# Kernel tuning notes

Measured on AMD Instinct MI355X. Metric: run time of the kernel, lower is better.

## Reference

```python
import jax, jax.numpy as jnp
import numpy as np

B, T, D_IN = 8192, 32, 2
EMB, H = 128, 256


def setup_inputs() -> dict:
    key = jax.random.key(0)
    ks = jax.random.split(key, 8)
    s = 0.05
    return {
        "traj_inputs": jax.random.normal(ks[0], (B, T, D_IN), dtype=jnp.float32),
        "W_emb": jax.random.normal(ks[1], (D_IN, EMB), dtype=jnp.float32) * s,
        "b_emb": jnp.zeros((EMB,), dtype=jnp.float32),
        "W0": jax.random.normal(ks[2], (EMB, 4 * H), dtype=jnp.float32) * s,
        "U0": jax.random.normal(ks[3], (H, 4 * H), dtype=jnp.float32) * s,
        "b0": jnp.zeros((4 * H,), dtype=jnp.float32),
        "W1": jax.random.normal(ks[4], (H, 4 * H), dtype=jnp.float32) * s,
        "U1": jax.random.normal(ks[5], (H, 4 * H), dtype=jnp.float32) * s,
        "b1": jnp.zeros((4 * H,), dtype=jnp.float32),
    }


def _lstm_layer(x_seq, W, U, b):
    # x_seq: [B, T, D]; Keras LSTMCell gate order i, f, g(c), o
    bsz = x_seq.shape[0]
    h0 = jnp.zeros((bsz, H), dtype=x_seq.dtype)
    c0 = jnp.zeros((bsz, H), dtype=x_seq.dtype)
    # precompute input projection for all timesteps (one big GEMM)
    xz = jnp.einsum("btd,dk->btk", x_seq, W) + b  # [B, T, 4H]

    def step(carry, xz_t):
        h, c = carry
        z = xz_t + h @ U
        i, f, g, o = jnp.split(z, 4, axis=-1)
        i = jax.nn.sigmoid(i)
        f = jax.nn.sigmoid(f)
        g = jnp.tanh(g)
        o = jax.nn.sigmoid(o)
        c = f * c + i * g
        h = o * jnp.tanh(c)
        return (h, c), h

    (h_f, c_f), ys = jax.lax.scan(step, (h0, c0), jnp.swapaxes(xz, 0, 1))
    return jnp.swapaxes(ys, 0, 1), h_f, c_f  # [B,T,H], [B,H], [B,H]


def reference(traj_inputs, W_emb, b_emb, W0, U0, b0, W1, U1, b1):
    # position embedding: Dense(emb_size, relu)
    x = jax.nn.relu(traj_inputs @ W_emb + b_emb)  # [B, T, EMB]
    # stacked 2-layer LSTM, return_sequences + return_state
    y0, h0, c0 = _lstm_layer(x, W0, U0, b0)
    y1, h1, c1 = _lstm_layer(y0, W1, U1, b1)
    # Keras RNN(StackedRNNCells) returns (seq_out, [h0,c0], [h1,c1])
    return y1, h0, c0, h1, c1
```

## Files before the change

kernel.cpp:

```cpp
#include <hip/hip_runtime.h>
#include <hip/hip_bf16.h>


typedef __attribute__((ext_vector_type(8))) __bf16 bf16x8;
typedef __attribute__((ext_vector_type(4))) __bf16 bf16x4;
typedef __attribute__((ext_vector_type(4))) float f32x4;

#define MFMA16(a, b, c) __builtin_amdgcn_mfma_f32_16x16x32_bf16(a, b, c, 0, 0, 0)

#define WAIT_VM3() __builtin_amdgcn_s_waitcnt(0xF73)
#define WAIT_LGKM0() __builtin_amdgcn_s_waitcnt(0xC07F)
#define RAW_BARRIER()                  \
  do {                                 \
    WAIT_LGKM0();                      \
    __builtin_amdgcn_sched_barrier(0); \
    __builtin_amdgcn_s_barrier();      \
  } while (0)

__device__ __forceinline__ float fexp2(float x) {
#if __has_builtin(__builtin_amdgcn_exp2f)
  return __builtin_amdgcn_exp2f(x);
#else
  return exp2f(x);
#endif
}
__device__ __forceinline__ float frcp(float x) {
#if __has_builtin(__builtin_amdgcn_rcpf)
  return __builtin_amdgcn_rcpf(x);
#else
  return 1.0f / x;
#endif
}
__device__ __forceinline__ float fsig(float x) {
  return frcp(1.0f + fexp2(-1.44269504f * x));
}
__device__ __forceinline__ float ftanh(float x) {
  return 1.0f - 2.0f * frcp(1.0f + fexp2(2.88539008f * x));
}

__global__ void prep_w0(const float* __restrict__ W0, const float* __restrict__ U0,
                        __bf16* __restrict__ o) {
  const int f = blockIdx.x * 256 + threadIdx.x;
  const int j = f & 7, l5 = (f >> 3) & 63, g = f >> 9;
  const int kc = g % 12, q = (g / 12) & 3, wid = g / 48;
  const int k = (kc << 5) + ((l5 >> 4) << 3) + j;
  const int c = (q << 8) + ((wid >> 2) << 6) + ((wid & 3) << 4) + (l5 & 15);
  const float v = (k < 128) ? W0[(k << 10) + c] : U0[((k - 128) << 10) + c];
  o[f] = (__bf16)v;
}
__global__ void prep_w1(const float* __restrict__ W1, const float* __restrict__ U1,
                        __bf16* __restrict__ o) {
  const int f = blockIdx.x * 256 + threadIdx.x;
  const int j = f & 7, l5 = (f >> 3) & 63, g = f >> 9;
  const int kcx = g & 15, q = (g >> 4) & 3, wid = g >> 6;
  const int k = (kcx << 5) + ((l5 >> 4) << 3) + j;
  const int c = (q << 8) + ((wid >> 2) << 6) + ((wid & 3) << 4) + (l5 & 15);
  const float v = (k < 256) ? W1[(k << 10) + c] : U1[((k - 256) << 10) + c];
  o[f] = (__bf16)v;
}

__global__ __launch_bounds__(1024)
void lstm_l0(const float* __restrict__ traj,
             const float* __restrict__ Wemb,
             const float* __restrict__ bemb,
             const float* __restrict__ bias0,
             const __bf16* __restrict__ wb0,
             float* __restrict__ out,
             __bf16* __restrict__ slab) {
  __shared__ float s_We[384];
  __shared__ float s_b[1024];
  __shared__ float s_traj[2048];
  __shared__ __bf16 s_h0[8192];
  __shared__ __bf16 s_ring[32768];

  const int tid = threadIdx.x;
  const int wid = tid >> 6;
  const int l = tid & 63;
  const int lr = l & 15, lg = l >> 4;
  const int w = wid >> 2, s4 = wid & 3;
  const int xr = (lr & 7) << 3;
  const int r0 = blockIdx.x << 5;
  const int e0 = (w << 6) + (s4 << 4) + (lg << 2);

  if (tid < 384) s_We[tid] = (tid < 256) ? Wemb[tid] : bemb[tid - 256];
  {
    const int ct = tid >> 4, cc = tid & 15;
    const int wd = ct >> 2, q = ct & 3;
    const int col = (q << 8) + ((wd >> 2) << 6) + ((wd & 3) << 4) + cc;
    s_b[tid] = bias0[col];
  }
  for (int i = tid; i < 2048; i += 1024) {
    const int r = i >> 6, tt = (i >> 1) & 31, d = i & 1;
    s_traj[(tt << 6) + (r << 1) + d] = traj[(r0 << 6) + i];
  }
  for (int i = tid; i < 8192; i += 1024) s_h0[i] = (__bf16)0.f;
  __syncthreads();

  float c0s[2][4] = {};
  const __bf16* wp0 = wb0 + wid * 48 * 512 + l * 8;
  __bf16* ringp = &s_ring[wid << 11];

  auto stage = [&](int cf) {
    const __bf16* src = wp0 + (((cf & 3) * 12 + (cf >> 2)) << 9);
    __builtin_amdgcn_global_load_lds(
        (const __attribute__((address_space(1))) void*)src,
        (__attribute__((address_space(3))) void*)(ringp + ((cf & 3) << 9)),
        16, 0, 0);
  };
  auto ring_read = [&](int cf) {
    return *reinterpret_cast<const bf16x8*>(ringp + ((cf & 3) << 9) + (l << 3));
  };

  stage(0); stage(1); stage(2);

#pragma unroll 1
  for (int t = 0; t < 32; ++t) {
    f32x4 acc[4][2];
#pragma unroll
    for (int q = 0; q < 4; ++q) {
      const f32x4 b =
          *reinterpret_cast<const f32x4*>(&s_b[(((wid << 2) + q) << 4) + (lg << 2)]);
      acc[q][0] = b;
      acc[q][1] = b;
    }
    float t0v[2], t1v[2];
#pragma unroll
    for (int rt = 0; rt < 2; ++rt) {
      const int r = (rt << 4) + lr;
      t0v[rt] = s_traj[(t << 6) + (r << 1)];
      t1v[rt] = s_traj[(t << 6) + (r << 1) + 1];
    }
#pragma unroll
    for (int kc = 0; kc < 12; ++kc) {
      bf16x8 ia[2];
      if (kc < 4) {
#pragma unroll
        for (int rt = 0; rt < 2; ++rt) {
#pragma unroll
          for (int j = 0; j < 8; ++j) {
            const int k = (kc << 5) + (lg << 3) + j;
            const float x = fmaf(t0v[rt], s_We[k],
                                 fmaf(t1v[rt], s_We[128 + k], s_We[256 + k]));
            ia[rt][j] = (__bf16)fmaxf(x, 0.f);
          }
        }
      } else {
#pragma unroll
        for (int rt = 0; rt < 2; ++rt) {
          const int r = (rt << 4) + lr;
          ia[rt] = *reinterpret_cast<const bf16x8*>(
              &s_h0[(r << 8) + ((((kc - 4) << 5) + (lg << 3)) ^ xr)]);
        }
      }
#pragma unroll
      for (int q = 0; q < 4; ++q) {
        const int cf = (kc << 2) + q;
        stage((cf + 3) % 48);
        WAIT_VM3();
        __builtin_amdgcn_sched_barrier(0);
        const bf16x8 wf = ring_read(cf);
        acc[q][0] = MFMA16(wf, ia[0], acc[q][0]);
        acc[q][1] = MFMA16(wf, ia[1], acc[q][1]);
      }
    }
    RAW_BARRIER();
#pragma unroll
    for (int rt = 0; rt < 2; ++rt) {
      const int r = (rt << 4) + lr;
      bf16x4 hv;
      f32x4 cfv;
#pragma unroll
      for (int i = 0; i < 4; ++i) {
        const float cc = fsig(acc[1][rt][i]) * c0s[rt][i] +
                         fsig(acc[0][rt][i]) * ftanh(acc[2][rt][i]);
        c0s[rt][i] = cc;
        hv[i] = (__bf16)(fsig(acc[3][rt][i]) * ftanh(cc));
        cfv[i] = cc;
      }
      *reinterpret_cast<bf16x4*>(&s_h0[(r << 8) + (e0 ^ xr)]) = hv;
      if (t == 31) {
        __builtin_nontemporal_store(
            cfv, reinterpret_cast<f32x4*>(out + 69206016 + ((r0 + r) << 8) + e0));
      }
    }
    RAW_BARRIER();

#pragma unroll
    for (int rr = 0; rr < 2; ++rr) {
      const int row = (wid << 1) + rr;
      const bf16x4 hv4 = *reinterpret_cast<const bf16x4*>(
          &s_h0[(row << 8) + ((l << 2) ^ ((row & 7) << 3))]);
      __builtin_nontemporal_store(
          hv4, reinterpret_cast<bf16x4*>(
                   slab + ((size_t)(t * 8192 + r0 + row) << 8) + (l << 2)));
      if (t == 31) {
        f32x4 v;
#pragma unroll
        for (int i = 0; i < 4; ++i) v[i] = (float)hv4[i];
        __builtin_nontemporal_store(
            v, reinterpret_cast<f32x4*>(out + 67108864 + ((r0 + row) << 8) + (l << 2)));
      }
    }
  }
}

__global__ __launch_bounds__(1024)
void lstm_l1(const float* __restrict__ bias1,
             const __bf16* __restrict__ wb1,
             const __bf16* __restrict__ slab,
             float* __restrict__ out) {
  __shared__ float s_b[1024];
  __shared__ __bf16 s_h0[8192];
  __shared__ __bf16 s_h1[8192];
  __shared__ __bf16 s_ring[32768];

  const int tid = threadIdx.x;
  const int wid = tid >> 6;
  const int l = tid & 63;
  const int lr = l & 15, lg = l >> 4;
  const int w = wid >> 2, s4 = wid & 3;
  const int xr = (lr & 7) << 3;
  const int r0 = blockIdx.x << 5;
  const int e0 = (w << 6) + (s4 << 4) + (lg << 2);

  {
    const int ct = tid >> 4, cc = tid & 15;
    const int wd = ct >> 2, q = ct & 3;
    const int col = (q << 8) + ((wd >> 2) << 6) + ((wd & 3) << 4) + cc;
    s_b[tid] = bias1[col];
  }
  for (int i = tid; i < 8192; i += 1024) s_h1[i] = (__bf16)0.f;
  __syncthreads();

  float c1s[2][4] = {};
  const __bf16* wp1 = wb1 + wid * 64 * 512 + l * 8;
  __bf16* ringp = &s_ring[wid << 11];

  auto stage = [&](int cf) {
    const int it8 = (cf >> 2) & 15, q = cf & 3;
    const int kcx = it8 ^ 8;
    const __bf16* src = wp1 + (((q << 4) + kcx) << 9);
    __builtin_amdgcn_global_load_lds(
        (const __attribute__((address_space(1))) void*)src,
        (__attribute__((address_space(3))) void*)(ringp + ((cf & 3) << 9)),
        16, 0, 0);
  };
  auto ring_read = [&](int cf) {
    return *reinterpret_cast<const bf16x8*>(ringp + ((cf & 3) << 9) + (l << 3));
  };

  const int irow = (wid << 1) + (l >> 5);
  const int iwb = (l & 31) << 4;
  const size_t ioff =
      ((size_t)(r0 + irow) << 8) + ((iwb ^ ((irow & 7) << 4)) >> 1);

  stage(0); stage(1); stage(2);

#pragma unroll 1
  for (int t = 0; t < 32; ++t) {
    __builtin_amdgcn_global_load_lds(
        (const __attribute__((address_space(1))) void*)(slab +
            (((size_t)t * 8192) << 8) + ioff),
        (__attribute__((address_space(3))) void*)(s_h0 + (wid << 9)),
        16, 0, 2);

    f32x4 acc[4][2];
#pragma unroll
    for (int q = 0; q < 4; ++q) {
      const f32x4 b =
          *reinterpret_cast<const f32x4*>(&s_b[(((wid << 2) + q) << 4) + (lg << 2)]);
      acc[q][0] = b;
      acc[q][1] = b;
    }
#pragma unroll
    for (int it8 = 0; it8 < 8; ++it8) {
      bf16x8 ib[2];
#pragma unroll
      for (int rt = 0; rt < 2; ++rt) {
        const int r = (rt << 4) + lr;
        ib[rt] = *reinterpret_cast<const bf16x8*>(
            &s_h1[(r << 8) + (((it8 << 5) + (lg << 3)) ^ xr)]);
      }
#pragma unroll
      for (int q = 0; q < 4; ++q) {
        const int cf = (it8 << 2) + q;
        stage((cf + 3) % 64);
        WAIT_VM3();
        __builtin_amdgcn_sched_barrier(0);
        const bf16x8 wf = ring_read(cf);
        acc[q][0] = MFMA16(wf, ib[0], acc[q][0]);
        acc[q][1] = MFMA16(wf, ib[1], acc[q][1]);
      }
    }
    RAW_BARRIER();
#pragma unroll
    for (int it8 = 8; it8 < 16; ++it8) {
      const int kcl = it8 - 8;
      bf16x8 ib[2];
#pragma unroll
      for (int rt = 0; rt < 2; ++rt) {
        const int r = (rt << 4) + lr;
        ib[rt] = *reinterpret_cast<const bf16x8*>(
            &s_h0[(r << 8) + (((kcl << 5) + (lg << 3)) ^ xr)]);
      }
#pragma unroll
      for (int q = 0; q < 4; ++q) {
        const int cf = (it8 << 2) + q;
        stage((cf + 3) % 64);
        WAIT_VM3();
        __builtin_amdgcn_sched_barrier(0);
        const bf16x8 wf = ring_read(cf);
        acc[q][0] = MFMA16(wf, ib[0], acc[q][0]);
        acc[q][1] = MFMA16(wf, ib[1], acc[q][1]);
      }
    }
    RAW_BARRIER();
#pragma unroll
    for (int rt = 0; rt < 2; ++rt) {
      const int r = (rt << 4) + lr;
      bf16x4 hv;
      f32x4 cfv;
#pragma unroll
      for (int i = 0; i < 4; ++i) {
        const float cc = fsig(acc[1][rt][i]) * c1s[rt][i] +
                         fsig(acc[0][rt][i]) * ftanh(acc[2][rt][i]);
        c1s[rt][i] = cc;
        hv[i] = (__bf16)(fsig(acc[3][rt][i]) * ftanh(cc));
        cfv[i] = cc;
      }
      *reinterpret_cast<bf16x4*>(&s_h1[(r << 8) + (e0 ^ xr)]) = hv;
      if (t == 31) {
        __builtin_nontemporal_store(
            cfv, reinterpret_cast<f32x4*>(out + 73400320 + ((r0 + r) << 8) + e0));
      }
    }
    RAW_BARRIER();

#pragma unroll
    for (int j = 0; j < 2; ++j) {
      const int row = (wid << 1) + j;
      const int xw = (row & 7) << 3;
      const bf16x4 a =
          *reinterpret_cast<const bf16x4*>(&s_h1[(row << 8) + ((l << 2) ^ xw)]);
      f32x4 v;
#pragma unroll
      for (int i = 0; i < 4; ++i) v[i] = (float)a[i];
      __builtin_nontemporal_store(
          v, reinterpret_cast<f32x4*>(out + ((((r0 + row) << 5) + t) << 8) + (l << 2)));
      if (t == 31) {
        __builtin_nontemporal_store(
            v, reinterpret_cast<f32x4*>(out + 71303168 + ((r0 + row) << 8) + (l << 2)));
      }
    }
  }
}

extern "C" void kernel_launch(void* const* d_in, const int* in_sizes, int n_in,
                              void* d_out, int out_size, void* d_ws, size_t ws_size,
                              hipStream_t stream) {
  const float* traj = (const float*)d_in[0];
  const float* Wemb = (const float*)d_in[1];
  const float* bemb = (const float*)d_in[2];
  const float* W0 = (const float*)d_in[3];
  const float* U0 = (const float*)d_in[4];
  const float* b0 = (const float*)d_in[5];
  const float* W1 = (const float*)d_in[6];
  const float* U1 = (const float*)d_in[7];
  const float* b1 = (const float*)d_in[8];
  float* out = (float*)d_out;

  __bf16* wb0 = (__bf16*)d_ws;
  __bf16* wb1 = wb0 + 393216;
  const size_t slab_off = 1835008;
  __bf16* slab = (__bf16*)((char*)d_ws + slab_off);

  hipLaunchKernelGGL(prep_w0, dim3(1536), dim3(256), 0, stream, W0, U0, wb0);
  hipLaunchKernelGGL(prep_w1, dim3(2048), dim3(256), 0, stream, W1, U1, wb1);
  hipLaunchKernelGGL(lstm_l0, dim3(256), dim3(1024), 0, stream,
                     traj, Wemb, bemb, b0, wb0, out, slab);
  hipLaunchKernelGGL(lstm_l1, dim3(256), dim3(1024), 0, stream,
                     b1, wb1, slab, out);
}
```

Before: 1.382 ms.

## Add cross-block group barriers per timestep to keep blocks in lockstep

Adds a per-timestep atomic-counter barrier across groups of 32 blocks, grouped by blockIdx mod 8, in both LSTM layer kernels. Each block waits until all 32 blocks in its group have reached the step. The aim is to keep blocks that share weight streams in lockstep so the weight loads hit in L2/MALL instead of drifting apart. The cost is atomic and spin overhead each step, plus a deadlock risk if all 256 blocks are not co-resident. A memset of the counters and a shifted workspace layout are also added.

```diff
diff --git a/kernel.cpp b/kernel.cpp
--- a/kernel.cpp
+++ b/kernel.cpp
@@ -15,6 +15,20 @@
     WAIT_LGKM0();                      \
     __builtin_amdgcn_sched_barrier(0); \
     __builtin_amdgcn_s_barrier();      \
+  } while (0)
+
+#define GROUP_BARRIER(cnt, t)                                              \
+  do {                                                                     \
+    if (threadIdx.x == 0) {                                                \
+      unsigned* slot = (cnt) + ((t) << 3) + (blockIdx.x & 7);              \
+      __hip_atomic_fetch_add(slot, 1u, __ATOMIC_RELAXED,                   \
+                             __HIP_MEMORY_SCOPE_AGENT);                    \
+      while (__hip_atomic_load(slot, __ATOMIC_RELAXED,                     \
+                               __HIP_MEMORY_SCOPE_AGENT) < 32u) {          \
+        __builtin_amdgcn_s_sleep(8);                                       \
+      }                                                                    \
+    }                                                                      \
+    __syncthreads();                                                       \
   } while (0)
 
 __device__ __forceinline__ float fexp2(float x) {
@@ -66,7 +80,8 @@
              const float* __restrict__ bias0,
              const __bf16* __restrict__ wb0,
              float* __restrict__ out,
-             __bf16* __restrict__ slab) {
+             __bf16* __restrict__ slab,
+             unsigned* __restrict__ cnt) {
   __shared__ float s_We[384];
   __shared__ float s_b[1024];
   __shared__ float s_traj[2048];
@@ -115,6 +130,8 @@
 
 #pragma unroll 1
   for (int t = 0; t < 32; ++t) {
+    if (t > 0) GROUP_BARRIER(cnt, t);
+
     f32x4 acc[4][2];
 #pragma unroll
     for (int q = 0; q < 4; ++q) {
@@ -208,7 +225,8 @@
 void lstm_l1(const float* __restrict__ bias1,
              const __bf16* __restrict__ wb1,
              const __bf16* __restrict__ slab,
-             float* __restrict__ out) {
+             float* __restrict__ out,
+             unsigned* __restrict__ cnt) {
   __shared__ float s_b[1024];
   __shared__ __bf16 s_h0[8192];
   __shared__ __bf16 s_h1[8192];
@@ -263,6 +281,8 @@
             (((size_t)t * 8192) << 8) + ioff),
         (__attribute__((address_space(3))) void*)(s_h0 + (wid << 9)),
         16, 0, 2);
+
+    if (t > 0) GROUP_BARRIER(cnt, t);
 
     f32x4 acc[4][2];
 #pragma unroll
@@ -371,13 +391,15 @@
 
   __bf16* wb0 = (__bf16*)d_ws;
   __bf16* wb1 = wb0 + 393216;
-  const size_t slab_off = 1835008;
-  __bf16* slab = (__bf16*)((char*)d_ws + slab_off);
-
+  unsigned* cnt0 = (unsigned*)((char*)d_ws + 1835008);
+  unsigned* cnt1 = cnt0 + 256;
+  __bf16* slab = (__bf16*)((char*)d_ws + 1837056);
+
+  hipMemsetAsync(cnt0, 0, 2048, stream);
   hipLaunchKernelGGL(prep_w0, dim3(1536), dim3(256), 0, stream, W0, U0, wb0);
   hipLaunchKernelGGL(prep_w1, dim3(2048), dim3(256), 0, stream, W1, U1, wb1);
   hipLaunchKernelGGL(lstm_l0, dim3(256), dim3(1024), 0, stream,
-                     traj, Wemb, bemb, b0, wb0, out, slab);
+                     traj, Wemb, bemb, b0, wb0, out, slab, cnt0);
   hipLaunchKernelGGL(lstm_l1, dim3(256), dim3(1024), 0, stream,
-                     b1, wb1, slab, out);
-}
+                     b1, wb1, slab, out, cnt1);
+}
```

Result: slower. 1.510 ms (+9.2%).
